# Performance work log

Hardware: AMD Instinct MI355X
Metric: run time of the kernel (lower is better)

The kernel has to match this reference:

```python
import jax, jax.numpy as jnp
import numpy as np

N_NODES = 100000


def _gcn_norm(edge_index, num_nodes):
    # add self loops, then symmetric normalization D^-1/2 (A+I) D^-1/2
    loops = jnp.arange(num_nodes, dtype=edge_index.dtype)
    src = jnp.concatenate([edge_index[0], loops])
    dst = jnp.concatenate([edge_index[1], loops])
    ones = jnp.ones(src.shape[0], dtype=jnp.float32)
    deg = jax.ops.segment_sum(ones, dst, num_segments=num_nodes)
    dinv = jnp.where(deg > 0, jax.lax.rsqrt(deg), 0.0)
    norm = dinv[src] * dinv[dst]  # [E+N]
    return src, dst, norm


def setup_inputs() -> dict:
    key = jax.random.key(0)
    k1, k2, k3, k4 = jax.random.split(key, 4)
    x = jax.random.normal(k1, (N_NODES, 512), dtype=jnp.float32)
    edge_index = jax.random.randint(k2, (2, 3200000), 0, N_NODES, dtype=jnp.int64)
    # SGConv linear: Linear(num_features=512, num_classes=40)
    W = jax.random.normal(k3, (40, 512), dtype=jnp.float32) / np.sqrt(512.0)
    b = jax.random.normal(k4, (40,), dtype=jnp.float32) * 0.01
    return {"x": x, "edge_index": edge_index, "W": W, "b": b}


def reference(x, edge_index, W, b):
    K = 2  # args.num_layers
    src, dst, norm = _gcn_norm(edge_index, N_NODES)
    h = x
    for _ in range(K):
        # SpMM: out[dst] += norm * h[src]
        h = jax.ops.segment_sum(norm[:, None] * h[src], dst, num_segments=N_NODES)
    logits = h @ W.T + b  # [N, num_classes]
    return jax.nn.log_softmax(logits, axis=1)
```

## Files before the change

kernel.cpp:

```cpp
#include <hip/hip_runtime.h>
#include <hip/hip_bf16.h>
#include <math.h>


#define NFEAT 512
#define NCLS  40
#define NBUCK_MAX 512
#define CAP   9728

typedef __attribute__((ext_vector_type(8))) short bf16x8;
typedef __attribute__((ext_vector_type(4))) float f32x4;

__device__ inline short f2bf(float f) {
    union { float f; unsigned u; } v; v.f = f;
    unsigned r = (v.u + 0x7FFFu + ((v.u >> 16) & 1u)) >> 16;
    return (short)r;
}
__device__ inline float bf2f(unsigned short u) {
    union { unsigned u; float f; } r; r.u = (unsigned)u << 16; return r.f;
}


__global__ __launch_bounds__(256) void scat7_kernel(const int* __restrict__ src,
                                                    const int* __restrict__ dst,
                                                    int* __restrict__ bcursor,
                                                    unsigned* __restrict__ bco, int E) {
    __shared__ int h[NBUCK_MAX], h2[NBUCK_MAX], base[NBUCK_MAX];
    int t = threadIdx.x;
    h[t] = 0; h[t + 256] = 0; h2[t] = 0; h2[t + 256] = 0;
    __syncthreads();
    int cb = blockIdx.x * 2048;
    int d[8], s[8];
    bool m[8];
    #pragma unroll
    for (int u = 0; u < 8; ++u) {
        int e = cb + u * 256 + t;
        m[u] = e < E;
        d[u] = m[u] ? __builtin_nontemporal_load(dst + e) : 0;
        s[u] = m[u] ? __builtin_nontemporal_load(src + e) : 0;
        if (m[u]) atomicAdd(&h[d[u] >> 8], 1);
    }
    __syncthreads();
    #pragma unroll
    for (int b = 0; b < 2; ++b) {
        int bb = t + b * 256;
        if (h[bb]) base[bb] = bb * CAP + atomicAdd(&bcursor[bb], h[bb]);
    }
    __syncthreads();
    #pragma unroll
    for (int u = 0; u < 8; ++u) {
        if (m[u]) {
            int b = d[u] >> 8;
            int lp = atomicAdd(&h2[b], 1);
            bco[base[b] + lp] = ((unsigned)s[u] << 8) | (unsigned)(d[u] & 255);
        }
    }
}


__global__ __launch_bounds__(256) void sortb3_kernel(const unsigned* __restrict__ bco,
                                                     const int* __restrict__ bcursor,
                                                     int4* __restrict__ rowinfo,
                                                     float* __restrict__ dinv,
                                                     int* __restrict__ csr_src, int N) {
    __shared__ int deg[256], ex[256], sc[256];
    int b = blockIdx.x, t = threadIdx.x;
    int lo = b * 256;
    int nn = N - lo; if (nn > 256) nn = 256;
    int ebeg = b * CAP;
    int ecnt = bcursor[b];

    deg[t] = 0;
    __syncthreads();
    for (int i = t; i < ecnt; i += 256)
        atomicAdd(&deg[bco[ebeg + i] & 255u], 1);
    __syncthreads();
    int v = deg[t];
    sc[t] = v;
    __syncthreads();
    for (int off = 1; off < 256; off <<= 1) {
        int u = (t >= off) ? sc[t - off] : 0;
        __syncthreads();
        sc[t] += u;
        __syncthreads();
    }
    int ext = sc[t] - v;
    ex[t] = ext;
    if (t < nn) {
        float di = rsqrtf((float)(v + 1));
        int4 ri;
        ri.x = ebeg + ext;
        ri.y = v;
        ri.z = __float_as_int(di);
        ri.w = 0;
        rowinfo[lo + t] = ri;
        dinv[lo + t]    = di;
    }
    __syncthreads();
    for (int i = t; i < ecnt; i += 256) {
        unsigned e = bco[ebeg + i];
        int p = atomicAdd(&ex[e & 255u], 1);
        csr_src[ebeg + p] = (int)(e >> 8);
    }
}


__global__ void wfrag_kernel(const float* __restrict__ W, short* __restrict__ wfrag) {
    int i = blockIdx.x * blockDim.x + threadIdx.x;
    if (i >= 16 * 3 * 64) return;
    int kc = i / 192, rem = i % 192, tile = rem / 64, lane = rem % 64;
    int c = tile * 16 + (lane & 15);
    int kbase = kc * 32 + ((lane >> 4) << 3);
    bf16x8 out;
    #pragma unroll
    for (int j = 0; j < 8; ++j) {
        float v = (c < NCLS) ? W[(size_t)c * NFEAT + kbase + j] : 0.f;
        out[j] = f2bf(v);
    }
    *(bf16x8*)(wfrag + (size_t)i * 8) = out;
}


__global__ __launch_bounds__(512) void gemm6_kernel(const float* __restrict__ x,
                                                    const short* __restrict__ wfrag,
                                                    const float* __restrict__ dinv,
                                                    unsigned short* __restrict__ zA,
                                                    unsigned short* __restrict__ zB, int n) {
    __shared__ short xl[2][128 * 40];
    int t = threadIdx.x;
    int w = t >> 6, l = t & 63;
    int lrow = l & 15, lk = l >> 4;
    int rowBase = blockIdx.x * 128;
    int srow = t >> 2, skq = t & 3;
    f32x4 acc0 = {0.f, 0.f, 0.f, 0.f}, acc1 = acc0, acc2 = acc0;
    const float* xrow = x + (size_t)(rowBase + srow) * NFEAT + skq * 8;
    bool srOK = (rowBase + srow) < n;
    int aoff = (w * 16 + lrow) * 40 + lk * 8;
    int doff = srow * 40 + skq * 8;

    {
        float4 v0 = make_float4(0.f, 0.f, 0.f, 0.f), v1 = v0;
        if (srOK) { const float4* xp = (const float4*)xrow; v0 = xp[0]; v1 = xp[1]; }
        bf16x8 bv;
        bv[0] = f2bf(v0.x); bv[1] = f2bf(v0.y); bv[2] = f2bf(v0.z); bv[3] = f2bf(v0.w);
        bv[4] = f2bf(v1.x); bv[5] = f2bf(v1.y); bv[6] = f2bf(v1.z); bv[7] = f2bf(v1.w);
        *(bf16x8*)&xl[0][doff] = bv;
    }
    __syncthreads();

    for (int kc = 0; kc < 16; ++kc) {
        int cur = kc & 1;
        float4 v0 = make_float4(0.f, 0.f, 0.f, 0.f), v1 = v0;
        if (kc < 15 && srOK) {
            const float4* xp = (const float4*)(xrow + (kc + 1) * 32);
            v0 = xp[0]; v1 = xp[1];
        }
        bf16x8 af = *(const bf16x8*)&xl[cur][aoff];
        const bf16x8* wf = (const bf16x8*)(wfrag + (size_t)kc * 3 * 64 * 8);
        bf16x8 b0 = wf[l];
        bf16x8 b1 = wf[64 + l];
        bf16x8 b2 = wf[128 + l];
        acc0 = __builtin_amdgcn_mfma_f32_16x16x32_bf16(af, b0, acc0, 0, 0, 0);
        acc1 = __builtin_amdgcn_mfma_f32_16x16x32_bf16(af, b1, acc1, 0, 0, 0);
        acc2 = __builtin_amdgcn_mfma_f32_16x16x32_bf16(af, b2, acc2, 0, 0, 0);
        if (kc < 15) {
            bf16x8 bv;
            bv[0] = f2bf(v0.x); bv[1] = f2bf(v0.y); bv[2] = f2bf(v0.z); bv[3] = f2bf(v0.w);
            bv[4] = f2bf(v1.x); bv[5] = f2bf(v1.y); bv[6] = f2bf(v1.z); bv[7] = f2bf(v1.w);
            *(bf16x8*)&xl[cur ^ 1][doff] = bv;
            __syncthreads();
        }
    }
    int r0 = rowBase + w * 16 + lk * 4;
    #pragma unroll
    for (int reg = 0; reg < 4; ++reg) {
        int row = r0 + reg;
        if (row < n) {
            float sc = dinv[row];
            unsigned short* zpA = zA + (size_t)row * 32;
            zpA[lrow]      = (unsigned short)f2bf(acc0[reg] * sc);
            zpA[16 + lrow] = (unsigned short)f2bf(acc1[reg] * sc);
            if (lrow < 8) zB[(size_t)row * 8 + lrow] = (unsigned short)f2bf(acc2[reg] * sc);
        }
    }
}


template <bool FINAL>
__global__ __launch_bounds__(256) void spmm8_kernel(const unsigned short* __restrict__ inA,
                                                    const unsigned short* __restrict__ inB,
                                                    const int4* __restrict__ rowinfo,
                                                    const int* __restrict__ csr,
                                                    const float* __restrict__ bias,
                                                    unsigned short* __restrict__ outA,
                                                    unsigned short* __restrict__ outB,
                                                    float* __restrict__ outF, int n) {
    int wv = (int)((blockIdx.x * (size_t)blockDim.x + threadIdx.x) >> 6);
    wv = __builtin_amdgcn_readfirstlane(wv);
    if (wv >= n) return;
    int lane = threadIdx.x & 63;
    bool lact = lane < NCLS;
    bool isA  = lane < 32;

    const char* lane_base = isA ? ((const char*)inA + lane * 2)
                                : ((const char*)inB + (lane - 32) * 2);
    unsigned lane_sh = isA ? 6u : 4u;

    int4 ri = rowinfo[wv];
    int beg = ri.x, tot = ri.y;
    float dd = __int_as_float(ri.z);

    float a = 0.f;
    if (lact) a = bf2f(*(const unsigned short*)(lane_base + ((size_t)wv << lane_sh)));

    int j = 0;
    for (; j + 4 <= tot; j += 4) {
        int s0 = csr[beg + j];
        int s1 = csr[beg + j + 1];
        int s2 = csr[beg + j + 2];
        int s3 = csr[beg + j + 3];
        if (lact) {
            float v0 = bf2f(*(const unsigned short*)(lane_base + ((size_t)s0 << lane_sh)));
            float v1 = bf2f(*(const unsigned short*)(lane_base + ((size_t)s1 << lane_sh)));
            float v2 = bf2f(*(const unsigned short*)(lane_base + ((size_t)s2 << lane_sh)));
            float v3 = bf2f(*(const unsigned short*)(lane_base + ((size_t)s3 << lane_sh)));
            a += v0; a += v1; a += v2; a += v3;
        }
    }
    for (; j < tot; ++j) {
        int s = csr[beg + j];
        if (lact) a += bf2f(*(const unsigned short*)(lane_base + ((size_t)s << lane_sh)));
    }

    if (!FINAL) {
        if (lact) {
            unsigned short o = (unsigned short)f2bf(a * dd * dd);
            if (isA) outA[(size_t)wv * 32 + lane] = o;
            else     outB[(size_t)wv * 8 + lane - 32] = o;
        }
    } else {
        float v = lact ? a * dd + bias[lane] : -INFINITY;
        float m = v;
        #pragma unroll
        for (int off = 32; off; off >>= 1) m = fmaxf(m, __shfl_xor(m, off, 64));
        float e = lact ? expf(v - m) : 0.f;
        float s = e;
        #pragma unroll
        for (int off = 32; off; off >>= 1) s += __shfl_xor(s, off, 64);
        float lse = logf(s);
        if (lact) outF[(size_t)wv * NCLS + lane] = v - m - lse;
    }
}


extern "C" void kernel_launch(void* const* d_in, const int* in_sizes, int n_in,
                              void* d_out, int out_size, void* d_ws, size_t ws_size,
                              hipStream_t stream) {
    const float* x  = (const float*)d_in[0];
    const int*   ei = (const int*)d_in[1];
    const float* W  = (const float*)d_in[2];
    const float* b  = (const float*)d_in[3];

    const int N = in_sizes[0] / NFEAT;
    const int E = in_sizes[1] / 2;
    const int* src = ei;
    const int* dst = ei + E;
    const int nbuck = (N + 255) >> 8;

    char* p = (char*)d_ws;
    auto alloc = [&](size_t bytes) -> void* {
        void* r = (void*)p;
        p += (bytes + 255) & ~(size_t)255;
        return r;
    };
    int*      bcursor = (int*)     alloc((size_t)NBUCK_MAX * 4);
    int4*     rowinfo = (int4*)    alloc((size_t)N * 16);
    float*    dinv    = (float*)   alloc((size_t)N * 4);
    unsigned* bco     = (unsigned*)alloc((size_t)nbuck * CAP * 4 + 64);
    int*      csr_src = (int*)     alloc((size_t)nbuck * CAP * 4 + 64);
    short*    wfrag   = (short*)   alloc((size_t)16 * 3 * 64 * 8 * 2);
    unsigned short* zA  = (unsigned short*)alloc((size_t)N * 32 * 2);
    unsigned short* zB  = (unsigned short*)alloc((size_t)N * 8 * 2);
    unsigned short* h1A = (unsigned short*)alloc((size_t)N * 32 * 2);
    unsigned short* h1B = (unsigned short*)alloc((size_t)N * 8 * 2);

    hipMemsetAsync(bcursor, 0, (size_t)NBUCK_MAX * 4, stream);

    int cb = (E + 2047) / 2048;
    scat7_kernel<<<cb, 256, 0, stream>>>(src, dst, bcursor, bco, E);
    sortb3_kernel<<<nbuck, 256, 0, stream>>>(bco, bcursor, rowinfo, dinv, csr_src, N);

    wfrag_kernel<<<12, 256, 0, stream>>>(W, wfrag);
    gemm6_kernel<<<(N + 127) / 128, 512, 0, stream>>>(x, wfrag, dinv, zA, zB, N);

    int wb = (int)(((size_t)N * 64 + 255) / 256);
    spmm8_kernel<false><<<wb, 256, 0, stream>>>(zA, zB, rowinfo, csr_src, b,
                                                h1A, h1B, nullptr, N);
    spmm8_kernel<true ><<<wb, 256, 0, stream>>>(h1A, h1B, rowinfo, csr_src, b,
                                                nullptr, nullptr, (float*)d_out, N);
}
```

Measured before the change: 302.1 us.

## Split SpMM wave into two half-waves gathering bf16 pairs over alternating edges

```diff
diff --git a/kernel.cpp b/kernel.cpp
--- a/kernel.cpp
+++ b/kernel.cpp
@@ -15,6 +15,15 @@
     union { float f; unsigned u; } v; v.f = f;
     unsigned r = (v.u + 0x7FFFu + ((v.u >> 16) & 1u)) >> 16;
     return (short)r;
+}
+__device__ inline unsigned pack2bf(float a, float b) {
+    return (unsigned)(unsigned short)f2bf(a) | ((unsigned)(unsigned short)f2bf(b) << 16);
+}
+__device__ inline float bflo(unsigned v) {
+    union { unsigned u; float f; } r; r.u = v << 16; return r.f;
+}
+__device__ inline float bfhi(unsigned v) {
+    union { unsigned u; float f; } r; r.u = v & 0xFFFF0000u; return r.f;
 }
 __device__ inline float bf2f(unsigned short u) {
     union { unsigned u; float f; } r; r.u = (unsigned)u << 16; return r.f;
@@ -105,8 +114,10 @@
 }
 
 
-__global__ void wfrag_kernel(const float* __restrict__ W, short* __restrict__ wfrag) {
+__global__ void wfrag_kernel(const float* __restrict__ W, short* __restrict__ wfrag,
+                             int* __restrict__ bcursor) {
     int i = blockIdx.x * blockDim.x + threadIdx.x;
+    if (i < NBUCK_MAX) bcursor[i] = 0;
     if (i >= 16 * 3 * 64) return;
     int kc = i / 192, rem = i % 192, tile = rem / 64, lane = rem % 64;
     int c = tile * 16 + (lane & 15);
@@ -187,68 +198,92 @@
 
 
 template <bool FINAL>
-__global__ __launch_bounds__(256) void spmm8_kernel(const unsigned short* __restrict__ inA,
-                                                    const unsigned short* __restrict__ inB,
-                                                    const int4* __restrict__ rowinfo,
-                                                    const int* __restrict__ csr,
-                                                    const float* __restrict__ bias,
-                                                    unsigned short* __restrict__ outA,
-                                                    unsigned short* __restrict__ outB,
-                                                    float* __restrict__ outF, int n) {
+__global__ __launch_bounds__(256) void spmm10_kernel(const unsigned short* __restrict__ inA,
+                                                     const unsigned short* __restrict__ inB,
+                                                     const int4* __restrict__ rowinfo,
+                                                     const int* __restrict__ csr,
+                                                     const float* __restrict__ bias,
+                                                     unsigned* __restrict__ outA,
+                                                     unsigned* __restrict__ outB,
+                                                     float* __restrict__ outF, int n) {
     int wv = (int)((blockIdx.x * (size_t)blockDim.x + threadIdx.x) >> 6);
     wv = __builtin_amdgcn_readfirstlane(wv);
     if (wv >= n) return;
     int lane = threadIdx.x & 63;
-    bool lact = lane < NCLS;
-    bool isA  = lane < 32;
-
-    const char* lane_base = isA ? ((const char*)inA + lane * 2)
-                                : ((const char*)inB + (lane - 32) * 2);
+    int hl = lane & 31, half = lane >> 5;
+    bool act = hl < (NCLS / 2);
+    bool isA = hl < 16;
+
+    const char* lane_base = isA ? ((const char*)inA + hl * 4)
+                                : ((const char*)inB + (hl - 16) * 4);
     unsigned lane_sh = isA ? 6u : 4u;
 
     int4 ri = rowinfo[wv];
     int beg = ri.x, tot = ri.y;
     float dd = __int_as_float(ri.z);
 
-    float a = 0.f;
-    if (lact) a = bf2f(*(const unsigned short*)(lane_base + ((size_t)wv << lane_sh)));
+    float a0 = 0.f, a1 = 0.f;
+    if (act && half == 0) {
+        unsigned v = *(const unsigned*)(lane_base + ((size_t)wv << lane_sh));
+        a0 = bflo(v); a1 = bfhi(v);
+    }
 
     int j = 0;
-    for (; j + 4 <= tot; j += 4) {
-        int s0 = csr[beg + j];
-        int s1 = csr[beg + j + 1];
-        int s2 = csr[beg + j + 2];
-        int s3 = csr[beg + j + 3];
-        if (lact) {
-            float v0 = bf2f(*(const unsigned short*)(lane_base + ((size_t)s0 << lane_sh)));
-            float v1 = bf2f(*(const unsigned short*)(lane_base + ((size_t)s1 << lane_sh)));
-            float v2 = bf2f(*(const unsigned short*)(lane_base + ((size_t)s2 << lane_sh)));
-            float v3 = bf2f(*(const unsigned short*)(lane_base + ((size_t)s3 << lane_sh)));
-            a += v0; a += v1; a += v2; a += v3;
-        }
-    }
-    for (; j < tot; ++j) {
+    for (; j + 32 <= tot; j += 32) {
+        int ss[32];
+        #pragma unroll
+        for (int u = 0; u < 32; ++u) ss[u] = csr[beg + j + u];
+        if (act) {
+            unsigned uu[16];
+            #pragma unroll
+            for (int u = 0; u < 16; ++u) {
+                int s = half ? ss[2 * u + 1] : ss[2 * u];
+                uu[u] = *(const unsigned*)(lane_base + ((size_t)s << lane_sh));
+            }
+            #pragma unroll
+            for (int u = 0; u < 16; ++u) { a0 += bflo(uu[u]); a1 += bfhi(uu[u]); }
+        }
+    }
+    for (; j + 2 <= tot; j += 2) {
+        int s0 = csr[beg + j], s1 = csr[beg + j + 1];
+        if (act) {
+            int s = half ? s1 : s0;
+            unsigned v = *(const unsigned*)(lane_base + ((size_t)s << lane_sh));
+            a0 += bflo(v); a1 += bfhi(v);
+        }
+    }
+    if (j < tot) {
         int s = csr[beg + j];
-        if (lact) a += bf2f(*(const unsigned short*)(lane_base + ((size_t)s << lane_sh)));
-    }
+        if (act && half == 0) {
+            unsigned v = *(const unsigned*)(lane_base + ((size_t)s << lane_sh));
+            a0 += bflo(v); a1 += bfhi(v);
+        }
+    }
+    a0 += __shfl_xor(a0, 32, 64);
+    a1 += __shfl_xor(a1, 32, 64);
 
     if (!FINAL) {
-        if (lact) {
-            unsigned short o = (unsigned short)f2bf(a * dd * dd);
-            if (isA) outA[(size_t)wv * 32 + lane] = o;
-            else     outB[(size_t)wv * 8 + lane - 32] = o;
+        if (act && half == 0) {
+            unsigned o = pack2bf(a0 * dd * dd, a1 * dd * dd);
+            if (isA) outA[(size_t)wv * 16 + hl] = o;
+            else     outB[(size_t)wv * 4 + (hl - 16)] = o;
         }
     } else {
-        float v = lact ? a * dd + bias[lane] : -INFINITY;
-        float m = v;
+        float2 bb = act ? ((const float2*)bias)[hl] : make_float2(0.f, 0.f);
+        float v0 = act ? a0 * dd + bb.x : -INFINITY;
+        float v1 = act ? a1 * dd + bb.y : -INFINITY;
+        float m = fmaxf(v0, v1);
         #pragma unroll
-        for (int off = 32; off; off >>= 1) m = fmaxf(m, __shfl_xor(m, off, 64));
-        float e = lact ? expf(v - m) : 0.f;
-        float s = e;
+        for (int off = 16; off; off >>= 1) m = fmaxf(m, __shfl_xor(m, off, 64));
+        float e0 = act ? expf(v0 - m) : 0.f;
+        float e1 = act ? expf(v1 - m) : 0.f;
+        float s = e0 + e1;
         #pragma unroll
-        for (int off = 32; off; off >>= 1) s += __shfl_xor(s, off, 64);
+        for (int off = 16; off; off >>= 1) s += __shfl_xor(s, off, 64);
         float lse = logf(s);
-        if (lact) outF[(size_t)wv * NCLS + lane] = v - m - lse;
+        if (act && half == 0)
+            *(float2*)(outF + (size_t)wv * NCLS + 2 * hl) =
+                make_float2(v0 - m - lse, v1 - m - lse);
     }
 }
 
@@ -284,18 +319,18 @@
     unsigned short* h1A = (unsigned short*)alloc((size_t)N * 32 * 2);
     unsigned short* h1B = (unsigned short*)alloc((size_t)N * 8 * 2);
 
-    hipMemsetAsync(bcursor, 0, (size_t)NBUCK_MAX * 4, stream);
+    wfrag_kernel<<<12, 256, 0, stream>>>(W, wfrag, bcursor);
 
     int cb = (E + 2047) / 2048;
     scat7_kernel<<<cb, 256, 0, stream>>>(src, dst, bcursor, bco, E);
     sortb3_kernel<<<nbuck, 256, 0, stream>>>(bco, bcursor, rowinfo, dinv, csr_src, N);
 
-    wfrag_kernel<<<12, 256, 0, stream>>>(W, wfrag);
     gemm6_kernel<<<(N + 127) / 128, 512, 0, stream>>>(x, wfrag, dinv, zA, zB, N);
 
     int wb = (int)(((size_t)N * 64 + 255) / 256);
-    spmm8_kernel<false><<<wb, 256, 0, stream>>>(zA, zB, rowinfo, csr_src, b,
-                                                h1A, h1B, nullptr, N);
-    spmm8_kernel<true ><<<wb, 256, 0, stream>>>(h1A, h1B, rowinfo, csr_src, b,
-                                                nullptr, nullptr, (float*)d_out, N);
-}
+    spmm10_kernel<false><<<wb, 256, 0, stream>>>(zA, zB, rowinfo, csr_src, b,
+                                                 (unsigned*)h1A, (unsigned*)h1B,
+                                                 nullptr, N);
+    spmm10_kernel<true ><<<wb, 256, 0, stream>>>(h1A, h1B, rowinfo, csr_src, b,
+                                                 nullptr, nullptr, (float*)d_out, N);
+}
```

New measurement: 444.5 us. +47.1%, slower.
